# Performance work log

Measured on AMD Instinct MI355X. Metric: run time of the kernel, lower is better.

Reference implementation:

```python
import jax, jax.numpy as jnp
import numpy as np
from jax import lax

B, T_TOK, H, T_MEL, K = 32, 1024, 256, 4096, 5


def setup_inputs() -> dict:
    key = jax.random.key(0)
    ks = jax.random.split(key, 16)
    x = jax.random.normal(ks[0], (B, T_TOK, H), jnp.float32)
    token_nums = jax.random.randint(ks[1], (B,), T_TOK // 2, T_TOK)
    # ground-truth per-token durations in mel frames (avg ~4 frames/token)
    mels_alignations = jax.random.uniform(ks[2], (B, T_TOK), jnp.float32) * 8.0
    mels_gt_num = jax.random.randint(ks[3], (B,), T_MEL // 2, T_MEL)
    s = 1.0 / np.sqrt(H * K)
    conv1_w = jax.random.uniform(ks[4], (H, H, K), jnp.float32, -s, s)
    conv1_b = jax.random.uniform(ks[5], (H,), jnp.float32, -s, s)
    ln1_g = jnp.ones((H,), jnp.float32)
    ln1_b = jnp.zeros((H,), jnp.float32)
    conv2_w = jax.random.uniform(ks[6], (H, H, K), jnp.float32, -s, s)
    conv2_b = jax.random.uniform(ks[7], (H,), jnp.float32, -s, s)
    ln2_g = jnp.ones((H,), jnp.float32)
    ln2_b = jnp.zeros((H,), jnp.float32)
    sl = 1.0 / np.sqrt(H)
    lin_w = jax.random.uniform(ks[8], (1, H), jnp.float32, -sl, sl)
    lin_b = jax.random.uniform(ks[9], (1,), jnp.float32, -sl, sl)
    return {"x": x, "token_nums": token_nums, "mels_alignations": mels_alignations,
            "mels_gt_num": mels_gt_num, "conv1_w": conv1_w, "conv1_b": conv1_b,
            "ln1_g": ln1_g, "ln1_b": ln1_b, "conv2_w": conv2_w, "conv2_b": conv2_b,
            "ln2_g": ln2_g, "ln2_b": ln2_b, "lin_w": lin_w, "lin_b": lin_b}


def conv1d_same(x, w, b):
    # x: [B, T, H] -> conv over T with kernel [H_out, H_in, K], padding SAME
    y = lax.conv_general_dilated(x.transpose(0, 2, 1), w, (1,), 'SAME',
                                 dimension_numbers=('NCH', 'OIH', 'NCH'))
    return y.transpose(0, 2, 1) + b


def layer_norm(x, g, b, eps=1e-5):
    mu = jnp.mean(x, axis=-1, keepdims=True)
    var = jnp.mean(jnp.square(x - mu), axis=-1, keepdims=True)
    return (x - mu) * lax.rsqrt(var + eps) * g + b


def reference(x, token_nums, mels_alignations, mels_gt_num,
              conv1_w, conv1_b, ln1_g, ln1_b,
              conv2_w, conv2_b, ln2_g, ln2_b, lin_w, lin_b):
    # NOTE: original forward computes the conv1/ln1/relu1 branch then overwrites
    # m with conv2(x) -- the conv1 branch does not affect outputs, so it is skipped.
    m = conv1d_same(x, conv2_w, conv2_b)                 # [B, T_TOK, H]
    m = jax.nn.relu(layer_norm(m, ln2_g, ln2_b))
    m = (m @ lin_w.T + lin_b)[..., 0]                    # [B, T_TOK]
    mask = jnp.arange(T_TOK)[None, :] < token_nums[:, None]
    m = jnp.where(mask, m, 0.0)                          # mels_alignations_predicted
    exp_m = jnp.where(mask, jnp.exp(m), 0.0)
    mels_num_predicted = exp_m.sum(axis=1).astype(jnp.int32)

    # expansion: running-clipped cumsum of gt durations -> frame->token map
    cum = jnp.minimum(jnp.cumsum(mels_alignations, axis=1),
                      mels_gt_num[:, None].astype(jnp.float32))  # [B, T_TOK]
    frames = jnp.arange(T_MEL, dtype=jnp.float32)
    tok = jax.vmap(lambda c: jnp.searchsorted(c, frames, side='right'))(cum)  # [B, T_MEL]
    valid = tok < T_TOK
    tok_c = jnp.minimum(tok, T_TOK - 1)
    x_new = jnp.where(valid[:, :, None],
                      jnp.take_along_axis(x, tok_c[:, :, None], axis=1), 0.0)
    return x_new, m, mels_num_predicted
```

## Files before the change

### kernel.cpp

```cpp
#include <hip/hip_runtime.h>
#include <hip/hip_bf16.h>

#define B_SZ 32
#define T_TOK 1024
#define H_DIM 256
#define T_MEL 4096
#define K_SZ 5
#define BM 64
#define ROWS (BM + 4)
#define XS_BYTES (ROWS * 512)
#define NCONV 512
#define NEXPB 512

typedef __attribute__((ext_vector_type(8))) short bf16x8;
typedef __attribute__((ext_vector_type(4))) float f32x4;

__device__ inline short f2bf(float f) {
    __hip_bfloat16 h = __float2bfloat16(f);
    return *reinterpret_cast<short*>(&h);
}

__global__ __launch_bounds__(256) void prep_kernel(const float* __restrict__ w,
                                                   short* __restrict__ wr,
                                                   const float* __restrict__ a,
                                                   const int* __restrict__ gt,
                                                   float* __restrict__ acc,
                                                   int* __restrict__ tokmap) {
    __shared__ float s_c[T_TOK];
    if (blockIdx.x < 160) {
        int idx = blockIdx.x * 256 + threadIdx.x;
        int lane = idx & 63;
        int n = (idx >> 6) & 15;
        int s = idx >> 10;
        int k = s >> 3;
        int hi0 = (s & 7) * 32 + (lane >> 4) * 8;
        int ho = n * 16 + (lane & 15);
        short out[8];
#pragma unroll
        for (int j = 0; j < 8; ++j)
            out[j] = f2bf(w[(ho * H_DIM + hi0 + j) * K_SZ + k]);
        *reinterpret_cast<bf16x8*>(wr + (size_t)idx * 8) = *reinterpret_cast<bf16x8*>(out);
        return;
    }
    int b = blockIdx.x - 160;
    int tid = threadIdx.x;
    if (tid == 1) acc[b] = 0.f;
    ((float4*)s_c)[tid] = ((const float4*)(a + b * T_TOK))[tid];
    __syncthreads();
    if (tid == 0) {
        float c = 0.f;
        float lim = (float)gt[b];
        for (int t = 0; t < T_TOK; ++t) {
            c += s_c[t];
            s_c[t] = fminf(c, lim);
        }
    }
    __syncthreads();
    int* tm = tokmap + b * T_MEL;
    for (int t = tid; t < T_TOK; t += 256) {
        float c1 = s_c[t];
        float c0 = (t == 0) ? 0.f : s_c[t - 1];
        int f0 = (int)ceilf(c0);
        int f1 = (int)ceilf(c1);
        for (int f = f0; f < f1; ++f) tm[f] = t;
    }
    int z0 = (int)ceilf(s_c[T_TOK - 1]);
    for (int f = z0 + tid; f < T_MEL; f += 256) tm[f] = T_TOK;
}

__global__ __launch_bounds__(512, 4) void fused_kernel(
    const float* __restrict__ x, const short* __restrict__ wr,
    const float* __restrict__ cb, const float* __restrict__ g,
    const float* __restrict__ beta, const float* __restrict__ lw,
    const float* __restrict__ lb, const int* __restrict__ tn,
    const int* __restrict__ tokmap,
    float* __restrict__ m_out, float* __restrict__ xnew, float* __restrict__ acc)
{
    __shared__ char smem[XS_BYTES];
    int tid = threadIdx.x;
    int lane = tid & 63;
    int wid = tid >> 6;

    if (blockIdx.x >= NCONV) {
        int e = blockIdx.x - NCONV;
        int fbase = e * 256;
        int b = e >> 4;
        int* s_tok = (int*)smem;
        if (tid < 256) s_tok[tid] = tokmap[fbase + tid];
        __syncthreads();
        const float* xb = x + (size_t)b * T_TOK * H_DIM;
        f32x4* dst = (f32x4*)(xnew + (size_t)(fbase + wid * 32) * H_DIM);
        f32x4 zv = {0.f, 0.f, 0.f, 0.f};
#pragma unroll
        for (int bt = 0; bt < 4; ++bt) {
            f32x4 v[8];
#pragma unroll
            for (int i = 0; i < 8; ++i) {
                int tok = s_tok[wid * 32 + bt * 8 + i];
                int tokc = min(tok, T_TOK - 1);
                v[i] = ((const f32x4*)(xb + (size_t)tokc * H_DIM))[lane];
                if (tok >= T_TOK) v[i] = zv;
            }
#pragma unroll
            for (int i = 0; i < 8; ++i)
                __builtin_nontemporal_store(v[i], dst + (bt * 8 + i) * 64 + lane);
        }
        return;
    }

    int b = blockIdx.x >> 4;
    int t0 = (blockIdx.x & 15) * BM;

    for (int i = tid; i < ROWS * 64; i += 512) {
        int row = i >> 6;
        int c4 = i & 63;
        int t = t0 - 2 + row;
        float4 v = make_float4(0.f, 0.f, 0.f, 0.f);
        if (t >= 0 && t < T_TOK)
            v = *reinterpret_cast<const float4*>(x + ((size_t)b * T_TOK + t) * H_DIM + c4 * 4);
        short4 h;
        h.x = f2bf(v.x); h.y = f2bf(v.y); h.z = f2bf(v.z); h.w = f2bf(v.w);
        int byte = row * 512 + c4 * 8;
        byte ^= (row & 7) << 4;
        *reinterpret_cast<short4*>(smem + byte) = h;
    }
    __syncthreads();

    const bf16x8* wf = reinterpret_cast<const bf16x8*>(wr);
    f32x4 zero = {0.f, 0.f, 0.f, 0.f};
    f32x4 acc_[4][2];
#pragma unroll
    for (int mi = 0; mi < 4; ++mi)
#pragma unroll
        for (int ni = 0; ni < 2; ++ni) acc_[mi][ni] = zero;

    int arow = lane & 15;
    int ccol = (lane >> 4) * 16;
    int n16 = wid * 2;

    bf16x8 bc[2], bn[2];
#pragma unroll
    for (int ni = 0; ni < 2; ++ni) bc[ni] = wf[(size_t)(n16 + ni) * 64 + lane];

    for (int s = 0; s < 40; ++s) {
        if (s < 39) {
#pragma unroll
            for (int ni = 0; ni < 2; ++ni)
                bn[ni] = wf[(size_t)((s + 1) * 16 + n16 + ni) * 64 + lane];
        }
        int rb = arow + (s >> 3);
        int cbase = (s & 7) * 64 + ccol;
        bf16x8 a[4];
#pragma unroll
        for (int mi = 0; mi < 4; ++mi) {
            int rr = mi * 16 + rb;
            int by = (rr * 512 + cbase) ^ ((rr & 7) << 4);
            a[mi] = *reinterpret_cast<const bf16x8*>(smem + by);
        }
#pragma unroll
        for (int mi = 0; mi < 4; ++mi)
#pragma unroll
            for (int ni = 0; ni < 2; ++ni)
                acc_[mi][ni] = __builtin_amdgcn_mfma_f32_16x16x32_bf16(a[mi], bc[ni], acc_[mi][ni], 0, 0, 0);
#pragma unroll
        for (int ni = 0; ni < 2; ++ni) bc[ni] = bn[ni];
    }

    __syncthreads();
    float* ps   = reinterpret_cast<float*>(smem);
    float* pq   = ps + 512;
    float* pdot = pq + 512;
    float* mus  = pdot + 512;
    float* rss  = mus + 64;

    float cbv[2];
#pragma unroll
    for (int ni = 0; ni < 2; ++ni) cbv[ni] = cb[wid * 32 + ni * 16 + (lane & 15)];

#pragma unroll
    for (int mi = 0; mi < 4; ++mi)
#pragma unroll
        for (int rr = 0; rr < 4; ++rr) {
            float s = 0.f, qq = 0.f;
#pragma unroll
            for (int ni = 0; ni < 2; ++ni) {
                float v = acc_[mi][ni][rr] + cbv[ni];
                s += v; qq += v * v;
            }
#pragma unroll
            for (int m = 1; m < 16; m <<= 1) {
                s += __shfl_xor(s, m);
                qq += __shfl_xor(qq, m);
            }
            if ((lane & 15) == 0) {
                int row = mi * 16 + (lane >> 4) * 4 + rr;
                ps[row * 8 + wid] = s;
                pq[row * 8 + wid] = qq;
            }
        }
    __syncthreads();
    if (tid < 64) {
        float S = 0.f, Q = 0.f;
#pragma unroll
        for (int w = 0; w < 8; ++w) { S += ps[tid * 8 + w]; Q += pq[tid * 8 + w]; }
        float mu = S * (1.f / 256.f);
        float var = Q * (1.f / 256.f) - mu * mu;
        mus[tid] = mu;
        rss[tid] = rsqrtf(var + 1e-5f);
    }
    __syncthreads();

    float gv[2], bv[2], lv[2];
#pragma unroll
    for (int ni = 0; ni < 2; ++ni) {
        int col = wid * 32 + ni * 16 + (lane & 15);
        gv[ni] = g[col]; bv[ni] = beta[col]; lv[ni] = lw[col];
    }
#pragma unroll
    for (int mi = 0; mi < 4; ++mi)
#pragma unroll
        for (int rr = 0; rr < 4; ++rr) {
            int row = mi * 16 + (lane >> 4) * 4 + rr;
            float mu = mus[row], rs = rss[row];
            float dt = 0.f;
#pragma unroll
            for (int ni = 0; ni < 2; ++ni) {
                float v = acc_[mi][ni][rr] + cbv[ni];
                float y = fmaxf((v - mu) * rs * gv[ni] + bv[ni], 0.f);
                dt += y * lv[ni];
            }
#pragma unroll
            for (int m = 1; m < 16; m <<= 1) dt += __shfl_xor(dt, m);
            if ((lane & 15) == 0) pdot[row * 8 + wid] = dt;
        }
    __syncthreads();
    if (tid < 64) {
        float dot = lb[0];
#pragma unroll
        for (int w = 0; w < 8; ++w) dot += pdot[tid * 8 + w];
        int t = t0 + tid;
        float mv = (t < tn[b]) ? dot : 0.f;
        m_out[b * T_TOK + t] = mv;
        float e = (t < tn[b]) ? expf(mv) : 0.f;
#pragma unroll
        for (int m = 1; m < 64; m <<= 1) e += __shfl_xor(e, m);
        if (tid == 0) atomicAdd(&acc[b], e);
    }
}

__global__ __launch_bounds__(64) void finalize_kernel(const float* __restrict__ acc,
                                                      float* __restrict__ out) {
    int b = threadIdx.x;
    if (b < B_SZ) out[b] = (float)((int)acc[b]);
}

extern "C" void kernel_launch(void* const* d_in, const int* in_sizes, int n_in,
                              void* d_out, int out_size, void* d_ws, size_t ws_size,
                              hipStream_t stream) {
    const float* x          = (const float*)d_in[0];
    const int*   token_nums = (const int*)d_in[1];
    const float* align      = (const float*)d_in[2];
    const int*   gt         = (const int*)d_in[3];
    const float* w2  = (const float*)d_in[8];
    const float* b2  = (const float*)d_in[9];
    const float* g2  = (const float*)d_in[10];
    const float* be2 = (const float*)d_in[11];
    const float* lw  = (const float*)d_in[12];
    const float* lb  = (const float*)d_in[13];

    float* out   = (float*)d_out;
    float* xnew  = out;
    float* m_out = out + (size_t)B_SZ * T_MEL * H_DIM;
    float* mels  = m_out + (size_t)B_SZ * T_TOK;

    short* wr   = (short*)d_ws;
    float* acc  = (float*)((char*)d_ws + (size_t)40 * 16 * 64 * 8 * 2);
    int* tokmap = (int*)((char*)acc + 128);

    prep_kernel<<<192, 256, 0, stream>>>(w2, wr, align, gt, acc, tokmap);
    fused_kernel<<<NCONV + NEXPB, 512, 0, stream>>>(x, wr, b2, g2, be2, lw, lb,
                                                    token_nums, tokmap, m_out, xnew, acc);
    finalize_kernel<<<1, 64, 0, stream>>>(acc, mels);
}
```

Before: 66.02 us.

## Split expansion gather into separate kernel and fold finalize into it

Moves the frame-expansion gather out of the fused conv kernel into its own kernel with 2048 smaller 256-thread blocks. Each wave handles 16 frames, broadcasting token indices by shuffle instead of staging them in shared memory. The stores are now regular rather than nontemporal. The finalize step is folded into the expand kernel, which removes one launch. The trade-off is that the gather no longer overlaps with the conv blocks, since the two now run as sequential kernels.

```diff
diff --git a/kernel.cpp b/kernel.cpp
--- a/kernel.cpp
+++ b/kernel.cpp
@@ -9,8 +9,6 @@
 #define BM 64
 #define ROWS (BM + 4)
 #define XS_BYTES (ROWS * 512)
-#define NCONV 512
-#define NEXPB 512
 
 typedef __attribute__((ext_vector_type(8))) short bf16x8;
 typedef __attribute__((ext_vector_type(4))) float f32x4;
@@ -68,46 +66,17 @@
     for (int f = z0 + tid; f < T_MEL; f += 256) tm[f] = T_TOK;
 }
 
-__global__ __launch_bounds__(512, 4) void fused_kernel(
+__global__ __launch_bounds__(512, 4) void conv_kernel(
     const float* __restrict__ x, const short* __restrict__ wr,
     const float* __restrict__ cb, const float* __restrict__ g,
     const float* __restrict__ beta, const float* __restrict__ lw,
     const float* __restrict__ lb, const int* __restrict__ tn,
-    const int* __restrict__ tokmap,
-    float* __restrict__ m_out, float* __restrict__ xnew, float* __restrict__ acc)
+    float* __restrict__ m_out, float* __restrict__ acc)
 {
     __shared__ char smem[XS_BYTES];
     int tid = threadIdx.x;
     int lane = tid & 63;
     int wid = tid >> 6;
-
-    if (blockIdx.x >= NCONV) {
-        int e = blockIdx.x - NCONV;
-        int fbase = e * 256;
-        int b = e >> 4;
-        int* s_tok = (int*)smem;
-        if (tid < 256) s_tok[tid] = tokmap[fbase + tid];
-        __syncthreads();
-        const float* xb = x + (size_t)b * T_TOK * H_DIM;
-        f32x4* dst = (f32x4*)(xnew + (size_t)(fbase + wid * 32) * H_DIM);
-        f32x4 zv = {0.f, 0.f, 0.f, 0.f};
-#pragma unroll
-        for (int bt = 0; bt < 4; ++bt) {
-            f32x4 v[8];
-#pragma unroll
-            for (int i = 0; i < 8; ++i) {
-                int tok = s_tok[wid * 32 + bt * 8 + i];
-                int tokc = min(tok, T_TOK - 1);
-                v[i] = ((const f32x4*)(xb + (size_t)tokc * H_DIM))[lane];
-                if (tok >= T_TOK) v[i] = zv;
-            }
-#pragma unroll
-            for (int i = 0; i < 8; ++i)
-                __builtin_nontemporal_store(v[i], dst + (bt * 8 + i) * 64 + lane);
-        }
-        return;
-    }
-
     int b = blockIdx.x >> 4;
     int t0 = (blockIdx.x & 15) * BM;
 
@@ -248,10 +217,36 @@
     }
 }
 
-__global__ __launch_bounds__(64) void finalize_kernel(const float* __restrict__ acc,
-                                                      float* __restrict__ out) {
-    int b = threadIdx.x;
-    if (b < B_SZ) out[b] = (float)((int)acc[b]);
+__global__ __launch_bounds__(256, 4) void expand_kernel(const float* __restrict__ x,
+                                                        const int* __restrict__ tokmap,
+                                                        const float* __restrict__ acc,
+                                                        float* __restrict__ xnew,
+                                                        float* __restrict__ mels) {
+    int tid = threadIdx.x;
+    int lane = tid & 63;
+    int wv = tid >> 6;
+    int fbase = (blockIdx.x * 4 + wv) * 16;
+    int b = fbase >> 12;
+
+    int tok16 = tokmap[fbase + (lane & 15)];
+    const f32x4* xb4 = (const f32x4*)x + (size_t)b * T_TOK * 64;
+    f32x4* dst4 = (f32x4*)xnew + (size_t)fbase * 64;
+    f32x4 zv = {0.f, 0.f, 0.f, 0.f};
+
+    f32x4 v[16];
+#pragma unroll
+    for (int i = 0; i < 16; ++i) {
+        int tok = __shfl(tok16, i, 16);
+        int tokc = min(tok, T_TOK - 1);
+        v[i] = xb4[(size_t)tokc * 64 + lane];
+        if (tok >= T_TOK) v[i] = zv;
+    }
+#pragma unroll
+    for (int i = 0; i < 16; ++i)
+        dst4[i * 64 + lane] = v[i];
+
+    if (blockIdx.x == 0 && tid < B_SZ)
+        mels[tid] = (float)((int)acc[tid]);
 }
 
 extern "C" void kernel_launch(void* const* d_in, const int* in_sizes, int n_in,
@@ -278,7 +273,7 @@
     int* tokmap = (int*)((char*)acc + 128);
 
     prep_kernel<<<192, 256, 0, stream>>>(w2, wr, align, gt, acc, tokmap);
-    fused_kernel<<<NCONV + NEXPB, 512, 0, stream>>>(x, wr, b2, g2, be2, lw, lb,
-                                                    token_nums, tokmap, m_out, xnew, acc);
-    finalize_kernel<<<1, 64, 0, stream>>>(acc, mels);
-}
+    conv_kernel<<<512, 512, 0, stream>>>(x, wr, b2, g2, be2, lw, lb,
+                                         token_nums, m_out, acc);
+    expand_kernel<<<2048, 256, 0, stream>>>(x, tokmap, acc, xnew, mels);
+}
```

Result: slower. 79.32 us (+20.1%).
